# Kernel optimization log

Hardware: AMD Instinct MI355X
Metric: run time of the kernel (lower is better)

Reference implementation:

```python
import jax, jax.numpy as jnp
import numpy as np

N = 100000
E = 1600000
D = 128


def setup_inputs() -> dict:
    key = jax.random.key(0)
    ks = jax.random.split(key, 16)
    inp = {
        "x": jax.random.normal(ks[0], (N, D), dtype=jnp.float32),
        "src": jax.random.randint(ks[1], (E,), 0, N, dtype=jnp.int32),
        "dst": jax.random.randint(ks[2], (E,), 0, N, dtype=jnp.int32),
    }
    scale = 1.0 / np.sqrt(D)
    for i in range(4):
        inp[f"ws{i}"] = jax.random.normal(ks[3 + 3 * i], (D, D), dtype=jnp.float32) * scale
        inp[f"wn{i}"] = jax.random.normal(ks[4 + 3 * i], (D, D), dtype=jnp.float32) * scale
        inp[f"b{i}"] = jnp.zeros((D,), dtype=jnp.float32)
    return inp


def _sage_layer(h, src, dst, w_self, w_neigh, b):
    # gather source-node features along edges, mean-reduce by destination
    msg = jnp.take(h, src, axis=0)                                   # [E, D]
    agg = jax.ops.segment_sum(msg, dst, num_segments=N)              # [N, D]
    deg = jax.ops.segment_sum(jnp.ones_like(dst, dtype=h.dtype), dst, num_segments=N)
    mean = agg / jnp.maximum(deg, 1.0)[:, None]                      # zero-degree -> 0
    return h @ w_self + mean @ w_neigh + b


def reference(x, src, dst, ws0, wn0, b0, ws1, wn1, b1, ws2, wn2, b2, ws3, wn3, b3):
    h = jax.nn.relu(_sage_layer(x, src, dst, ws0, wn0, b0))
    h = jax.nn.relu(_sage_layer(h, src, dst, ws1, wn1, b1))
    h = jax.nn.relu(_sage_layer(h, src, dst, ws2, wn2, b2))
    h = _sage_layer(h, src, dst, ws3, wn3, b3)
    return h
```

## Files before the change

kernel.cpp:

```cpp
#include <hip/hip_runtime.h>

#define N_NODES 100000
#define N_EDGES 1600000
#define DIM 128

typedef __attribute__((ext_vector_type(8))) _Float16 f16x8;
typedef __attribute__((ext_vector_type(4))) float f32x4;

__device__ __forceinline__ void stage16(const _Float16* g, _Float16* l) {
  __builtin_amdgcn_global_load_lds(
      (const __attribute__((address_space(1))) void*)g,
      (__attribute__((address_space(3))) void*)l, 16, 0, 0);
}


__global__ void k_zero(int* __restrict__ p, int n) {
  int i = blockIdx.x * blockDim.x + threadIdx.x;
  if (i < n) p[i] = 0;
}

__global__ void k_count(const int* __restrict__ dst, int* __restrict__ cnt) {
  int i = blockIdx.x * blockDim.x + threadIdx.x;
  if (i < N_EDGES) atomicAdd(&cnt[dst[i]], 1);
}

__global__ void k_scan_blk(const int* __restrict__ cnt, int* __restrict__ offs,
                           int* __restrict__ partials) {
  int tid = threadIdx.x;
  int gid = blockIdx.x * 1024 + tid;
  int v = (gid < N_NODES) ? cnt[gid] : 0;
  int lane = tid & 63, w = tid >> 6;
  int s = v;
#pragma unroll
  for (int d = 1; d < 64; d <<= 1) {
    int t = __shfl_up(s, d);
    if (lane >= d) s += t;
  }
  __shared__ int wsum[16];
  if (lane == 63) wsum[w] = s;
  __syncthreads();
  if (tid < 16) {
    int t2 = wsum[tid];
#pragma unroll
    for (int d = 1; d < 16; d <<= 1) {
      int u = __shfl_up(t2, d);
      if (tid >= d) t2 += u;
    }
    wsum[tid] = t2;
  }
  __syncthreads();
  if (w > 0) s += wsum[w - 1];
  if (gid < N_NODES) offs[gid + 1] = s;
  if (tid == 1023) partials[blockIdx.x] = s;
}

__global__ void k_scan_part(int* __restrict__ partials, int nb) {
  __shared__ int tmp[128];
  int tid = threadIdx.x;
  tmp[tid] = (tid < nb) ? partials[tid] : 0;
  __syncthreads();
  for (int d = 1; d < 128; d <<= 1) {
    int t = (tid >= d) ? tmp[tid - d] : 0;
    __syncthreads();
    tmp[tid] += t;
    __syncthreads();
  }
  if (tid < nb) partials[tid] = (tid > 0) ? tmp[tid - 1] : 0;
}

__global__ void k_scan_add(int* __restrict__ offs, const int* __restrict__ partials) {
  int i = blockIdx.x * blockDim.x + threadIdx.x;
  if (i == 0) offs[0] = 0;
  if (i < N_NODES) offs[i + 1] += partials[i >> 10];
}

__global__ void k_prep(const int* __restrict__ offs, const int* __restrict__ cnt,
                       int* __restrict__ cursor, float* __restrict__ deg_inv) {
  int i = blockIdx.x * blockDim.x + threadIdx.x;
  if (i < N_NODES) {
    cursor[i] = offs[i];
    deg_inv[i] = 1.0f / (float)max(cnt[i], 1);
  }
}

#define FILL_BPP 224
__global__ void k_fill8(const int* __restrict__ src, const int* __restrict__ dst,
                        int* __restrict__ cursor, int* __restrict__ esrc) {
  const int part = blockIdx.x & 7;
  const int bp = blockIdx.x >> 3;
  const int lo = part * (N_NODES / 8);
  const int hi = lo + (N_NODES / 8);
  for (int i = bp * 256 + threadIdx.x; i < N_EDGES; i += FILL_BPP * 256) {
    int d = dst[i];
    if (d >= lo && d < hi) {
      int p = atomicAdd(&cursor[d], 1);
      esrc[p] = src[i];
    }
  }
}


__global__ void k_xcvt(const float* __restrict__ x, _Float16* __restrict__ x1,
                       _Float16* __restrict__ x2) {
  int i = blockIdx.x * blockDim.x + threadIdx.x;
  if (i < (N_NODES * DIM) / 4) {
    float4 v = reinterpret_cast<const float4*>(x)[i];
    union { _Float16 h[4]; uint2 u; } a, b;
    float vv[4] = {v.x, v.y, v.z, v.w};
#pragma unroll
    for (int j = 0; j < 4; ++j) {
      _Float16 h1 = (_Float16)vv[j];
      a.h[j] = h1;
      b.h[j] = (_Float16)(vv[j] - (float)h1);
    }
    reinterpret_cast<uint2*>(x1)[i] = a.u;
    reinterpret_cast<uint2*>(x2)[i] = b.u;
  }
}


#define WP_LAYER (4 * 4 * 8 * 64 * 8)
#define WP_MAT (4 * 8 * 64 * 8)

__global__ void k_wpack(const float* __restrict__ ws0, const float* __restrict__ wn0,
                        const float* __restrict__ ws1, const float* __restrict__ wn1,
                        const float* __restrict__ ws2, const float* __restrict__ wn2,
                        const float* __restrict__ ws3, const float* __restrict__ wn3,
                        _Float16* __restrict__ wp) {
  int tid = blockIdx.x * 256 + threadIdx.x;
  int l = tid & 63;
  int f = (tid >> 6) & 7;
  int t = (tid >> 9) & 3;
  int m = (tid >> 11) & 3;
  int layer = tid >> 13;
  const float* srcs[8] = {ws0, wn0, ws1, wn1, ws2, wn2, ws3, wn3};
  const float* src = srcs[layer * 2 + (m >> 1)];
  int isLo = m & 1;
  _Float16* dstp = wp + (size_t)layer * WP_LAYER + ((((m * 4 + t) * 8 + f) * 64 + l) * 8);
  int k0 = t * 32 + (l >> 4) * 8;
  int col = f * 16 + (l & 15);
#pragma unroll
  for (int j = 0; j < 8; ++j) {
    float v = src[(k0 + j) * DIM + col];
    _Float16 h1 = (_Float16)v;
    dstp[j] = isLo ? (_Float16)(v - (float)h1) : h1;
  }
}


__device__ __forceinline__ float f16lo(unsigned w) {
  union { unsigned u; _Float16 h[2]; } c;
  c.u = w;
  return (float)c.h[0];
}
__device__ __forceinline__ float f16hi(unsigned w) {
  union { unsigned u; _Float16 h[2]; } c;
  c.u = w;
  return (float)c.h[1];
}

__global__ void k_agg_f16(const _Float16* __restrict__ h1, const int* __restrict__ offs,
                          const int* __restrict__ esrc, const float* __restrict__ deg_inv,
                          _Float16* __restrict__ m1) {
  int wid = (blockIdx.x * blockDim.x + threadIdx.x) >> 6;
  int lane = threadIdx.x & 63;
  if (wid >= N_NODES) return;
  const unsigned* H = reinterpret_cast<const unsigned*>(h1);
  int beg = offs[wid], end = offs[wid + 1];
  float xs[8] = {0.f, 0.f, 0.f, 0.f, 0.f, 0.f, 0.f, 0.f};
  float ys[8] = {0.f, 0.f, 0.f, 0.f, 0.f, 0.f, 0.f, 0.f};
  int e = beg;
  for (; e + 7 < end; e += 8) {
    int s[8];
#pragma unroll
    for (int j = 0; j < 8; ++j) s[j] = esrc[e + j];
    unsigned w[8];
#pragma unroll
    for (int j = 0; j < 8; ++j) w[j] = H[(size_t)s[j] * 64 + lane];
#pragma unroll
    for (int j = 0; j < 8; ++j) {
      xs[j] += f16lo(w[j]);
      ys[j] += f16hi(w[j]);
    }
  }
  for (; e + 1 < end; e += 2) {
    unsigned w0 = H[(size_t)esrc[e] * 64 + lane];
    unsigned w1 = H[(size_t)esrc[e + 1] * 64 + lane];
    xs[0] += f16lo(w0); ys[0] += f16hi(w0);
    xs[1] += f16lo(w1); ys[1] += f16hi(w1);
  }
  if (e < end) {
    unsigned w0 = H[(size_t)esrc[e] * 64 + lane];
    xs[2] += f16lo(w0); ys[2] += f16hi(w0);
  }
  float di = deg_inv[wid];
  float rx = ((xs[0] + xs[1]) + (xs[2] + xs[3])) + ((xs[4] + xs[5]) + (xs[6] + xs[7]));
  float ry = ((ys[0] + ys[1]) + (ys[2] + ys[3])) + ((ys[4] + ys[5]) + (ys[6] + ys[7]));
  rx *= di;
  ry *= di;
  union { unsigned u; _Float16 h[2]; } o;
  o.h[0] = (_Float16)rx;
  o.h[1] = (_Float16)ry;
  reinterpret_cast<unsigned*>(m1)[(size_t)wid * 64 + lane] = o.u;
}


template <int RELU, int LAST>
__global__ __launch_bounds__(256, 3) void k_gemm_f16(
    const _Float16* __restrict__ hp1, const _Float16* __restrict__ hp2,
    const _Float16* __restrict__ mp1, const _Float16* __restrict__ wp,
    const float* __restrict__ bias, float* __restrict__ outf,
    _Float16* __restrict__ o1, _Float16* __restrict__ o2) {
  __shared__ _Float16 sA[3][64 * 128];

  const int tid = threadIdx.x;
  const int lane = tid & 63;
  const int wv = tid >> 6;
  const int wr = wv >> 1;
  const int wc = wv & 1;
  const int row0 = blockIdx.x * 64;
  const int lr = lane & 15;
  const int lg = lane >> 4;

  const _Float16* planes[3] = {hp1, hp2, mp1};

#pragma unroll
  for (int p = 0; p < 3; ++p)
#pragma unroll
    for (int i = 0; i < 4; ++i) {
      int s = i * 256 + tid;
      int row = s >> 4;
      int chunk = (s & 15) ^ (row & 7);
      const _Float16* g = planes[p] + (size_t)(row0 + row) * DIM + chunk * 8;
      _Float16* l = &sA[p][(size_t)(i * 256 + (tid & ~63)) * 8];
      stage16(g, l);
    }
  __syncthreads();

  f32x4 acc[2][4];
#pragma unroll
  for (int i = 0; i < 2; ++i)
#pragma unroll
    for (int j = 0; j < 4; ++j) acc[i][j] = (f32x4){0.f, 0.f, 0.f, 0.f};

  const _Float16* WS1 = wp;
  const _Float16* WS2 = wp + WP_MAT;
  const _Float16* WN1 = wp + 2 * WP_MAT;
  const _Float16* WN2 = wp + 3 * WP_MAT;

#pragma unroll
  for (int t = 0; t < 4; ++t) {
    f16x8 a1[2], a2[2], am[2];
#pragma unroll
    for (int ri = 0; ri < 2; ++ri) {
      int row_l = wr * 32 + ri * 16 + lr;
      int boff = (row_l << 8) + ((t * 64 + lg * 16) ^ ((row_l & 7) << 4));
      a1[ri] = *reinterpret_cast<const f16x8*>(
          reinterpret_cast<const char*>(&sA[0][0]) + boff);
      a2[ri] = *reinterpret_cast<const f16x8*>(
          reinterpret_cast<const char*>(&sA[1][0]) + boff);
      am[ri] = *reinterpret_cast<const f16x8*>(
          reinterpret_cast<const char*>(&sA[2][0]) + boff);
    }
#pragma unroll
    for (int fc = 0; fc < 4; ++fc) {
      int f = wc * 4 + fc;
      size_t boff = (size_t)((t * 8 + f) * 64 + lane) * 8;
      f16x8 bs1 = *reinterpret_cast<const f16x8*>(WS1 + boff);
      f16x8 bs2 = *reinterpret_cast<const f16x8*>(WS2 + boff);
      f16x8 bn1 = *reinterpret_cast<const f16x8*>(WN1 + boff);
      f16x8 bn2 = *reinterpret_cast<const f16x8*>(WN2 + boff);
#pragma unroll
      for (int ri = 0; ri < 2; ++ri) {
        acc[ri][fc] =
            __builtin_amdgcn_mfma_f32_16x16x32_f16(a1[ri], bs1, acc[ri][fc], 0, 0, 0);
        acc[ri][fc] =
            __builtin_amdgcn_mfma_f32_16x16x32_f16(a2[ri], bs1, acc[ri][fc], 0, 0, 0);
        acc[ri][fc] =
            __builtin_amdgcn_mfma_f32_16x16x32_f16(a1[ri], bs2, acc[ri][fc], 0, 0, 0);
        acc[ri][fc] =
            __builtin_amdgcn_mfma_f32_16x16x32_f16(am[ri], bn1, acc[ri][fc], 0, 0, 0);
        acc[ri][fc] =
            __builtin_amdgcn_mfma_f32_16x16x32_f16(am[ri], bn2, acc[ri][fc], 0, 0, 0);
      }
    }
  }

  float bv[4];
#pragma unroll
  for (int fc = 0; fc < 4; ++fc) bv[fc] = bias[wc * 64 + fc * 16 + lr];
#pragma unroll
  for (int ri = 0; ri < 2; ++ri)
#pragma unroll
    for (int fc = 0; fc < 4; ++fc)
#pragma unroll
      for (int r = 0; r < 4; ++r) {
        int row = row0 + wr * 32 + ri * 16 + lg * 4 + r;
        if (row < N_NODES) {
          float v = acc[ri][fc][r] + bv[fc];
          if (RELU) v = fmaxf(v, 0.f);
          size_t idx = (size_t)row * DIM + wc * 64 + fc * 16 + lr;
          if (LAST) {
            outf[idx] = v;
          } else {
            _Float16 hi = (_Float16)v;
            o1[idx] = hi;
            o2[idx] = (_Float16)(v - (float)hi);
          }
        }
      }
}


extern "C" void kernel_launch(void* const* d_in, const int* in_sizes, int n_in,
                              void* d_out, int out_size, void* d_ws, size_t ws_size,
                              hipStream_t stream) {
  const float* x = (const float*)d_in[0];
  const int* src = (const int*)d_in[1];
  const int* dst = (const int*)d_in[2];
  const float* Ws[4];
  const float* Wn[4];
  const float* Bi[4];
  for (int i = 0; i < 4; ++i) {
    Ws[i] = (const float*)d_in[3 + 3 * i];
    Wn[i] = (const float*)d_in[4 + 3 * i];
    Bi[i] = (const float*)d_in[5 + 3 * i];
  }
  float* out = (float*)d_out;

  char* p = (char*)d_ws;
  auto take = [&](size_t bytes) {
    void* r = (void*)p;
    p += (bytes + 255) & ~(size_t)255;
    return r;
  };
  int* cnt = (int*)take((size_t)N_NODES * 4);
  int* offs = (int*)take((size_t)(N_NODES + 1) * 4);
  int* cursor = (int*)take((size_t)N_NODES * 4);
  int* partials = (int*)take(128 * 4);
  float* deg_inv = (float*)take((size_t)N_NODES * 4);
  int* esrc = (int*)take((size_t)N_EDGES * 4);
  _Float16* hA1 = (_Float16*)take((size_t)N_NODES * DIM * 2);
  _Float16* hA2 = (_Float16*)take((size_t)N_NODES * DIM * 2);
  _Float16* hB1 = (_Float16*)take((size_t)N_NODES * DIM * 2);
  _Float16* hB2 = (_Float16*)take((size_t)N_NODES * DIM * 2);
  _Float16* m1 = (_Float16*)take((size_t)N_NODES * DIM * 2);
  _Float16* wpk = (_Float16*)take((size_t)4 * WP_LAYER * 2);
  (void)take((size_t)64 * 1024);

  const int NB = (N_NODES + 1023) / 1024;

  k_zero<<<(N_NODES + 255) / 256, 256, 0, stream>>>(cnt, N_NODES);
  k_count<<<(N_EDGES + 255) / 256, 256, 0, stream>>>(dst, cnt);
  k_scan_blk<<<NB, 1024, 0, stream>>>(cnt, offs, partials);
  k_scan_part<<<1, 128, 0, stream>>>(partials, NB);
  k_scan_add<<<(N_NODES + 255) / 256, 256, 0, stream>>>(offs, partials);
  k_prep<<<(N_NODES + 255) / 256, 256, 0, stream>>>(offs, cnt, cursor, deg_inv);
  k_fill8<<<8 * FILL_BPP, 256, 0, stream>>>(src, dst, cursor, esrc);

  k_xcvt<<<(N_NODES * DIM / 4 + 255) / 256, 256, 0, stream>>>(x, hA1, hA2);
  k_wpack<<<128, 256, 0, stream>>>(Ws[0], Wn[0], Ws[1], Wn[1], Ws[2], Wn[2], Ws[3], Wn[3],
                                   wpk);

  const int AGG_BLOCKS = (N_NODES + 3) / 4;
  const int GEMM_BLOCKS = (N_NODES + 63) / 64;

  _Float16 *h1 = hA1, *h2 = hA2, *n1 = hB1, *n2 = hB2;
  for (int l = 0; l < 4; ++l) {
    k_agg_f16<<<AGG_BLOCKS, 256, 0, stream>>>(h1, offs, esrc, deg_inv, m1);
    const _Float16* wl = wpk + (size_t)l * WP_LAYER;
    if (l < 3) {
      k_gemm_f16<1, 0><<<GEMM_BLOCKS, 256, 0, stream>>>(h1, h2, m1, wl, Bi[l], nullptr,
                                                        n1, n2);
      _Float16* t1 = h1; h1 = n1; n1 = t1;
      _Float16* t2 = h2; h2 = n2; n2 = t2;
    } else {
      k_gemm_f16<0, 1><<<GEMM_BLOCKS, 256, 0, stream>>>(h1, h2, m1, wl, Bi[l], out,
                                                        nullptr, nullptr);
    }
  }
}
```

Before: 583.4 us.

## Drop weight low-half split in GEMM and fuse preprocessing kernels into one launch

Weights are now stored as a single fp16 plane instead of a hi/lo split pair, which removes two of the five MFMAs and two B-operand loads per inner step in the layer GEMM. The zero-count, input fp16 hi/lo conversion and weight packing kernels are merged into one launch, selected by block index, to save launch gaps. Activations still keep the hi/lo split. Dropping the weight residual lowers GEMM accuracy, with fp16 rounding error on the weights, which may matter for tolerance.

```diff
diff --git a/kernel.cpp b/kernel.cpp
--- a/kernel.cpp
+++ b/kernel.cpp
@@ -13,11 +13,6 @@
       (__attribute__((address_space(3))) void*)l, 16, 0, 0);
 }
 
-
-__global__ void k_zero(int* __restrict__ p, int n) {
-  int i = blockIdx.x * blockDim.x + threadIdx.x;
-  if (i < n) p[i] = 0;
-}
 
 __global__ void k_count(const int* __restrict__ dst, int* __restrict__ cnt) {
   int i = blockIdx.x * blockDim.x + threadIdx.x;
@@ -100,50 +95,54 @@
 }
 
 
-__global__ void k_xcvt(const float* __restrict__ x, _Float16* __restrict__ x1,
-                       _Float16* __restrict__ x2) {
-  int i = blockIdx.x * blockDim.x + threadIdx.x;
-  if (i < (N_NODES * DIM) / 4) {
-    float4 v = reinterpret_cast<const float4*>(x)[i];
-    union { _Float16 h[4]; uint2 u; } a, b;
-    float vv[4] = {v.x, v.y, v.z, v.w};
-#pragma unroll
-    for (int j = 0; j < 4; ++j) {
-      _Float16 h1 = (_Float16)vv[j];
-      a.h[j] = h1;
-      b.h[j] = (_Float16)(vv[j] - (float)h1);
-    }
-    reinterpret_cast<uint2*>(x1)[i] = a.u;
-    reinterpret_cast<uint2*>(x2)[i] = b.u;
-  }
-}
-
-
-#define WP_LAYER (4 * 4 * 8 * 64 * 8)
 #define WP_MAT (4 * 8 * 64 * 8)
-
-__global__ void k_wpack(const float* __restrict__ ws0, const float* __restrict__ wn0,
-                        const float* __restrict__ ws1, const float* __restrict__ wn1,
-                        const float* __restrict__ ws2, const float* __restrict__ wn2,
-                        const float* __restrict__ ws3, const float* __restrict__ wn3,
-                        _Float16* __restrict__ wp) {
-  int tid = blockIdx.x * 256 + threadIdx.x;
-  int l = tid & 63;
-  int f = (tid >> 6) & 7;
-  int t = (tid >> 9) & 3;
-  int m = (tid >> 11) & 3;
-  int layer = tid >> 13;
-  const float* srcs[8] = {ws0, wn0, ws1, wn1, ws2, wn2, ws3, wn3};
-  const float* src = srcs[layer * 2 + (m >> 1)];
-  int isLo = m & 1;
-  _Float16* dstp = wp + (size_t)layer * WP_LAYER + ((((m * 4 + t) * 8 + f) * 64 + l) * 8);
-  int k0 = t * 32 + (l >> 4) * 8;
-  int col = f * 16 + (l & 15);
-#pragma unroll
-  for (int j = 0; j < 8; ++j) {
-    float v = src[(k0 + j) * DIM + col];
-    _Float16 h1 = (_Float16)v;
-    dstp[j] = isLo ? (_Float16)(v - (float)h1) : h1;
+#define WP_LAYER (2 * WP_MAT)
+
+#define NZ_BLOCKS ((N_NODES + 255) / 256)
+#define NX_BLOCKS ((N_NODES * DIM / 4 + 255) / 256)
+#define NW_BLOCKS 64
+
+__global__ void k_preproc(int* __restrict__ cnt, const float* __restrict__ x,
+                          _Float16* __restrict__ x1, _Float16* __restrict__ x2,
+                          const float* __restrict__ ws0, const float* __restrict__ wn0,
+                          const float* __restrict__ ws1, const float* __restrict__ wn1,
+                          const float* __restrict__ ws2, const float* __restrict__ wn2,
+                          const float* __restrict__ ws3, const float* __restrict__ wn3,
+                          _Float16* __restrict__ wp) {
+  const int bid = blockIdx.x;
+  if (bid < NZ_BLOCKS) {
+    int i = bid * 256 + threadIdx.x;
+    if (i < N_NODES) cnt[i] = 0;
+  } else if (bid < NZ_BLOCKS + NX_BLOCKS) {
+    int i = (bid - NZ_BLOCKS) * 256 + threadIdx.x;
+    if (i < (N_NODES * DIM) / 4) {
+      float4 v = reinterpret_cast<const float4*>(x)[i];
+      union { _Float16 h[4]; uint2 u; } a, b;
+      float vv[4] = {v.x, v.y, v.z, v.w};
+#pragma unroll
+      for (int j = 0; j < 4; ++j) {
+        _Float16 h1 = (_Float16)vv[j];
+        a.h[j] = h1;
+        b.h[j] = (_Float16)(vv[j] - (float)h1);
+      }
+      reinterpret_cast<uint2*>(x1)[i] = a.u;
+      reinterpret_cast<uint2*>(x2)[i] = b.u;
+    }
+  } else {
+    int tid = (bid - NZ_BLOCKS - NX_BLOCKS) * 256 + threadIdx.x;
+    int l = tid & 63;
+    int f = (tid >> 6) & 7;
+    int t = (tid >> 9) & 3;
+    int m = (tid >> 11) & 1;
+    int layer = tid >> 12;
+    const float* srcs[8] = {ws0, wn0, ws1, wn1, ws2, wn2, ws3, wn3};
+    const float* src = srcs[layer * 2 + m];
+    _Float16* dstp =
+        wp + (size_t)layer * WP_LAYER + ((((m * 4 + t) * 8 + f) * 64 + l) * 8);
+    int k0 = t * 32 + (l >> 4) * 8;
+    int col = f * 16 + (l & 15);
+#pragma unroll
+    for (int j = 0; j < 8; ++j) dstp[j] = (_Float16)src[(k0 + j) * DIM + col];
   }
 }
 
@@ -244,9 +243,7 @@
     for (int j = 0; j < 4; ++j) acc[i][j] = (f32x4){0.f, 0.f, 0.f, 0.f};
 
   const _Float16* WS1 = wp;
-  const _Float16* WS2 = wp + WP_MAT;
-  const _Float16* WN1 = wp + 2 * WP_MAT;
-  const _Float16* WN2 = wp + 3 * WP_MAT;
+  const _Float16* WN1 = wp + WP_MAT;
 
 #pragma unroll
   for (int t = 0; t < 4; ++t) {
@@ -267,9 +264,7 @@
       int f = wc * 4 + fc;
       size_t boff = (size_t)((t * 8 + f) * 64 + lane) * 8;
       f16x8 bs1 = *reinterpret_cast<const f16x8*>(WS1 + boff);
-      f16x8 bs2 = *reinterpret_cast<const f16x8*>(WS2 + boff);
       f16x8 bn1 = *reinterpret_cast<const f16x8*>(WN1 + boff);
-      f16x8 bn2 = *reinterpret_cast<const f16x8*>(WN2 + boff);
 #pragma unroll
       for (int ri = 0; ri < 2; ++ri) {
         acc[ri][fc] =
@@ -277,11 +272,7 @@
         acc[ri][fc] =
             __builtin_amdgcn_mfma_f32_16x16x32_f16(a2[ri], bs1, acc[ri][fc], 0, 0, 0);
         acc[ri][fc] =
-            __builtin_amdgcn_mfma_f32_16x16x32_f16(a1[ri], bs2, acc[ri][fc], 0, 0, 0);
-        acc[ri][fc] =
             __builtin_amdgcn_mfma_f32_16x16x32_f16(am[ri], bn1, acc[ri][fc], 0, 0, 0);
-        acc[ri][fc] =
-            __builtin_amdgcn_mfma_f32_16x16x32_f16(am[ri], bn2, acc[ri][fc], 0, 0, 0);
       }
     }
   }
@@ -350,17 +341,15 @@
 
   const int NB = (N_NODES + 1023) / 1024;
 
-  k_zero<<<(N_NODES + 255) / 256, 256, 0, stream>>>(cnt, N_NODES);
+  k_preproc<<<NZ_BLOCKS + NX_BLOCKS + NW_BLOCKS, 256, 0, stream>>>(
+      cnt, x, hA1, hA2, Ws[0], Wn[0], Ws[1], Wn[1], Ws[2], Wn[2], Ws[3], Wn[3], wpk);
+
   k_count<<<(N_EDGES + 255) / 256, 256, 0, stream>>>(dst, cnt);
   k_scan_blk<<<NB, 1024, 0, stream>>>(cnt, offs, partials);
   k_scan_part<<<1, 128, 0, stream>>>(partials, NB);
   k_scan_add<<<(N_NODES + 255) / 256, 256, 0, stream>>>(offs, partials);
   k_prep<<<(N_NODES + 255) / 256, 256, 0, stream>>>(offs, cnt, cursor, deg_inv);
   k_fill8<<<8 * FILL_BPP, 256, 0, stream>>>(src, dst, cursor, esrc);
-
-  k_xcvt<<<(N_NODES * DIM / 4 + 255) / 256, 256, 0, stream>>>(x, hA1, hA2);
-  k_wpack<<<128, 256, 0, stream>>>(Ws[0], Wn[0], Ws[1], Wn[1], Ws[2], Wn[2], Ws[3], Wn[3],
-                                   wpk);
 
   const int AGG_BLOCKS = (N_NODES + 3) / 4;
   const int GEMM_BLOCKS = (N_NODES + 63) / 64;
```

After: 552.4 us. 1.06x faster.
